# Kernel optimization log

Measured on AMD Instinct MI355X. Metric: run time of the kernel, lower is better.

## Reference

```python
import jax, jax.numpy as jnp
import numpy as np
import math

NEG_INF = -1e9  # finite sentinel, safe under fp16/bf16 too


def _maximum_path(neg_x_ent):
    """Monotonic alignment search (VITS maximum_path), batched & wavefront-parallel.

    neg_x_ent: (B, T_feats, T_text) float32. Full lengths assumed (masks all ones).
    Returns hard path (B, T_feats, T_text) in {0,1}.
    """
    B, Tf, Tt = neg_x_ent.shape
    xs_idx = jnp.arange(Tt)

    # ---- forward DP: value[y, x] = max(value[y-1, x] (x!=y), value[y-1, x-1]) + neg[y, x]
    def fwd_step(prev, inputs):
        y, row = inputs  # y scalar, row (B, Tt)
        left0 = jnp.where(y == 0, 0.0, NEG_INF)  # v_prev for x==0
        v_left = jnp.concatenate(
            [jnp.broadcast_to(left0, (B, 1)), prev[:, :-1]], axis=1)
        v_cur = jnp.where(xs_idx[None, :] == y, NEG_INF, prev)
        val = jnp.maximum(v_cur, v_left) + row
        return val, val

    init = jnp.full((B, Tt), NEG_INF, dtype=neg_x_ent.dtype)
    _, values = jax.lax.scan(
        fwd_step, init, (jnp.arange(Tf), jnp.transpose(neg_x_ent, (1, 0, 2))))
    # values: (Tf, B, Tt); values_prev[y] = values[y-1] (row -1 is -inf)
    values_prev = jnp.concatenate(
        [jnp.full((1, B, Tt), NEG_INF, values.dtype), values[:-1]], axis=0)

    # ---- backtracking from (Tf-1, Tt-1)
    def back_step(idx, inputs):
        y, vprev = inputs  # idx (B,), vprev (B, Tt)
        onehot = (xs_idx[None, :] == idx[:, None]).astype(neg_x_ent.dtype)
        v_at = jnp.take_along_axis(vprev, idx[:, None], axis=1)[:, 0]
        v_lf = jnp.take_along_axis(
            vprev, jnp.maximum(idx - 1, 0)[:, None], axis=1)[:, 0]
        move = (idx != 0) & ((idx == y) | (v_at < v_lf))
        return idx - move.astype(idx.dtype), onehot

    idx0 = jnp.full((B,), Tt - 1, dtype=jnp.int32)
    _, path_rev = jax.lax.scan(
        back_step, idx0, (jnp.arange(Tf)[::-1], values_prev[::-1]))
    path = jnp.transpose(path_rev[::-1], (1, 0, 2))  # (B, Tf, Tt)
    return path


def reference(z_p, m_p, logs_p, x_mask, y_mask):
    # Gaussian negative cross-entropy between flow latent z_p and prior (m_p, logs_p)
    s_p_sq_r = jnp.exp(-2.0 * logs_p)                              # (B, C, Tt)
    neg1 = jnp.sum(-0.5 * math.log(2.0 * math.pi) - logs_p,
                   axis=1, keepdims=True)                          # (B, 1, Tt)
    neg2 = jnp.einsum('bct,bcs->bts', -0.5 * z_p ** 2, s_p_sq_r)   # (B, Tf, Tt)
    neg3 = jnp.einsum('bct,bcs->bts', z_p, m_p * s_p_sq_r)         # (B, Tf, Tt)
    neg4 = jnp.sum(-0.5 * m_p ** 2 * s_p_sq_r, axis=1, keepdims=True)
    neg_x_ent = neg1 + neg2 + neg3 + neg4                          # (B, Tf, Tt)

    attn_mask = x_mask[:, 0, None, :] * y_mask[:, 0, :, None]      # (B, Tf, Tt)
    attn = _maximum_path(neg_x_ent) * attn_mask                    # (B, Tf, Tt)
    dur = jnp.sum(attn, axis=1)                                    # (B, Tt)
    return attn, dur, neg_x_ent


def setup_inputs() -> dict:
    key = jax.random.key(0)
    k1, k2, k3 = jax.random.split(key, 3)
    B, C, Tf, Tt = 32, 192, 2048, 512
    return {
        'z_p': jax.random.normal(k1, (B, C, Tf), dtype=jnp.float32),
        'm_p': jax.random.normal(k2, (B, C, Tt), dtype=jnp.float32),
        'logs_p': jax.random.normal(k3, (B, C, Tt), dtype=jnp.float32),
        'x_mask': jnp.ones((B, 1, Tt), dtype=jnp.float32),
        'y_mask': jnp.ones((B, 1, Tf), dtype=jnp.float32),
    }
```

## Files before the change

kernel.cpp:

```cpp
#include <hip/hip_runtime.h>
#include <math.h>

#define BATCH 32
#define CH    192
#define TFEAT 2048
#define TTXT  512
#define NEGINF (-1e9f)

#define ATTN_ELEMS ((size_t)BATCH * TFEAT * TTXT)
#define DUR_OFF    ATTN_ELEMS
#define NEG_OFF    (ATTN_ELEMS + (size_t)BATCH * TTXT)

typedef short bf16x8 __attribute__((ext_vector_type(8)));
typedef float f32x16 __attribute__((ext_vector_type(16)));

__device__ __forceinline__ void gload_lds16h(const unsigned short* g,
                                             unsigned short* l) {
  __builtin_amdgcn_global_load_lds(
      (const __attribute__((address_space(1))) void*)g,
      (__attribute__((address_space(3))) void*)l, 16, 0, 0);
}

#define VMCNT(n) asm volatile("s_waitcnt vmcnt(" #n ")" ::: "memory")

__device__ __forceinline__ unsigned short f2b16(float f) {
  unsigned u = __float_as_uint(f);
  return (unsigned short)((u + 0x7FFFu + ((u >> 16) & 1u)) >> 16);
}

__global__ __launch_bounds__(256)
void k_transA(const float* __restrict__ z_p, unsigned short* __restrict__ At2) {
  __shared__ float zt[CH][33];
  int b = blockIdx.x >> 6, tblk = blockIdx.x & 63;
  int tid = threadIdx.x;
  int t0 = tblk * 32;
  for (int i = tid; i < CH * 32; i += 256) {
    int c = i >> 5, m = i & 31;
    zt[c][m] = z_p[((size_t)b * CH + c) * TFEAT + t0 + m];
  }
  __syncthreads();
  unsigned short* out = At2 + (size_t)(b * 64 + tblk) * 24 * 512;
  for (int o = tid; o < 24 * 512; o += 256) {
    int kq = o >> 9, rem = o & 511;
    int lane = rem >> 3, j = rem & 7;
    int m = lane & 31, kh = lane >> 5;
    int k = kq * 16 + kh * 8 + j;
    float f;
    if (k < CH) f = zt[k][m];
    else { float z = zt[k - CH][m]; f = z * z; }
    out[o] = f2b16(f);
  }
}

__global__ __launch_bounds__(256)
void k_transB(const float* __restrict__ m_p, const float* __restrict__ logs_p,
              unsigned short* __restrict__ Bt2) {
  __shared__ float w1t[CH][33];
  __shared__ float w2t[CH][33];
  int b = blockIdx.x >> 4, sblk = blockIdx.x & 15;
  int tid = threadIdx.x;
  int s0 = sblk * 32;
  for (int i = tid; i < CH * 32; i += 256) {
    int c = i >> 5, n = i & 31;
    size_t idx = ((size_t)b * CH + c) * TTXT + s0 + n;
    float m = m_p[idx];
    float r = __expf(-2.0f * logs_p[idx]);
    w1t[c][n] = m * r;
    w2t[c][n] = -0.5f * r;
  }
  __syncthreads();
  unsigned short* out = Bt2 + (size_t)(b * 16 + sblk) * 24 * 512;
  for (int o = tid; o < 24 * 512; o += 256) {
    int kq = o >> 9, rem = o & 511;
    int lane = rem >> 3, j = rem & 7;
    int n = lane & 31, kh = lane >> 5;
    int k = kq * 16 + kh * 8 + j;
    float f = (k < CH) ? w1t[k][n] : w2t[k - CH][n];
    out[o] = f2b16(f);
  }
}

__global__ void k_cadd(const float* __restrict__ m_p,
                       const float* __restrict__ logs_p,
                       float* __restrict__ cadd) {
  int gid = blockIdx.x * 256 + threadIdx.x;
  int b = gid >> 9, s = gid & (TTXT - 1);
  const float* mp = m_p    + (size_t)b * CH * TTXT + s;
  const float* lp = logs_p + (size_t)b * CH * TTXT + s;
  float acc = -0.5f * 1.8378770664093453f * (float)CH;
  #pragma unroll 4
  for (int c = 0; c < CH; ++c) {
    float l = lp[(size_t)c * TTXT];
    float m = mp[(size_t)c * TTXT];
    float r = __expf(-2.0f * l);
    acc -= l + 0.5f * m * m * r;
  }
  cadd[gid] = acc;
}

__global__ __launch_bounds__(512)
void k_mf(const unsigned short* __restrict__ At2,
          const unsigned short* __restrict__ Bt2,
          const float* __restrict__ cadd,
          float* __restrict__ neg,
          unsigned short* __restrict__ negh) {
  int blk = (blockIdx.x & 7) * 128 + (blockIdx.x >> 3);
  int sb = blk & 1;
  int tb = (blk >> 1) & 15;
  int b  = blk >> 5;
  int tid = threadIdx.x, lane = tid & 63, w = tid >> 6;
  int rg = w >> 2, cg = w & 3;
  int trow0 = tb * 128 + rg * 64;
  int scol0 = sb * 256 + cg * 64;

  const unsigned short* ap0 = At2 + ((size_t)(b * 64 + (trow0 >> 5)) * 24) * 512 + lane * 8;
  const unsigned short* ap1 = ap0 + (size_t)24 * 512;
  const unsigned short* bp0 = Bt2 + ((size_t)(b * 16 + (scol0 >> 5)) * 24) * 512 + lane * 8;
  const unsigned short* bp1 = bp0 + (size_t)24 * 512;

  f32x16 acc00, acc01, acc10, acc11;
  #pragma unroll
  for (int r = 0; r < 16; ++r) { acc00[r] = 0.f; acc01[r] = 0.f; acc10[r] = 0.f; acc11[r] = 0.f; }

  bf16x8 a0A, a1A, b0A, b1A;
  bf16x8 a0B, a1B, b0B, b1B;

  auto LDA = [&](bf16x8& x0, bf16x8& x1, bf16x8& y0, bf16x8& y1, int kq) {
    x0 = *(const bf16x8*)(ap0 + (size_t)kq * 512);
    x1 = *(const bf16x8*)(ap1 + (size_t)kq * 512);
    y0 = *(const bf16x8*)(bp0 + (size_t)kq * 512);
    y1 = *(const bf16x8*)(bp1 + (size_t)kq * 512);
  };
  auto FMA = [&](bf16x8& x0, bf16x8& x1, bf16x8& y0, bf16x8& y1) {
    acc00 = __builtin_amdgcn_mfma_f32_32x32x16_bf16(x0, y0, acc00, 0, 0, 0);
    acc01 = __builtin_amdgcn_mfma_f32_32x32x16_bf16(x0, y1, acc01, 0, 0, 0);
    acc10 = __builtin_amdgcn_mfma_f32_32x32x16_bf16(x1, y0, acc10, 0, 0, 0);
    acc11 = __builtin_amdgcn_mfma_f32_32x32x16_bf16(x1, y1, acc11, 0, 0, 0);
  };

  LDA(a0A, a1A, b0A, b1A, 0);
  #pragma unroll
  for (int kq = 0; kq < 24; kq += 2) {
    LDA(a0B, a1B, b0B, b1B, kq + 1);
    FMA(a0A, a1A, b0A, b1A);
    __builtin_amdgcn_sched_barrier(0);
    if (kq + 2 < 24) LDA(a0A, a1A, b0A, b1A, kq + 2);
    FMA(a0B, a1B, b0B, b1B);
    __builtin_amdgcn_sched_barrier(0);
  }

  #pragma unroll
  for (int ti = 0; ti < 2; ++ti) {
    #pragma unroll
    for (int tj = 0; tj < 2; ++tj) {
      const f32x16& v = (ti == 0) ? ((tj == 0) ? acc00 : acc01)
                                  : ((tj == 0) ? acc10 : acc11);
      int s = scol0 + tj * 32 + (lane & 31);
      float cv = cadd[b * TTXT + s];
      int tB = trow0 + ti * 32 + 4 * (lane >> 5);
      float* np_ = neg + (size_t)b * TFEAT * TTXT + s;
      #pragma unroll
      for (int r = 0; r < 16; ++r) {
        int t = tB + (r & 3) + 8 * (r >> 2);
        float o = v[r] + cv;
        np_[(size_t)t * TTXT] = o;
        negh[(((size_t)b * 128 + (t >> 4)) * 8 + (s >> 6)) * 1024
             + (t & 15) * 64 + (s & 63)] = f2b16(o);
      }
    }
  }
}

#define KROWS 16
#define NWIN  (TFEAT / KROWS)
#define NMASKW (TTXT / KROWS)

__device__ __forceinline__ float dpp_shr1(float v) {
  return __int_as_float(__builtin_amdgcn_update_dpp(
      __float_as_int(v), __float_as_int(v), 0x138 , 0xF, 0xF, false));
}

__global__ __launch_bounds__(512, 1)
void k_dp(const unsigned short* __restrict__ negh, float* __restrict__ dur,
          int* __restrict__ idx_out, const float* __restrict__ x_mask,
          unsigned long long* __restrict__ gbits_all) {
  __shared__ unsigned short ringh[8][4][KROWS * 64];
  __shared__ float bndlds[3][8][KROWS];
  int b = blockIdx.x, tid = threadIdx.x;
  int lane = tid & 63, w = tid >> 6;
  const unsigned short* nb =
      negh + (((size_t)b * NWIN) * 8 + w) * 1024 + lane * 8;
  unsigned long long* gbits = gbits_all + (size_t)b * 8 * TFEAT;

  if (tid < 3 * 8 * KROWS) ((float*)bndlds)[tid] = NEGINF;

  auto stage = [&](int j) {
    int slot = j & 3;
    const unsigned short* s0 = nb + (size_t)j * 8 * 1024;
    gload_lds16h(s0,       &ringh[w][slot][0]);
    gload_lds16h(s0 + 512, &ringh[w][slot][512]);
  };

  stage(0); stage(1); stage(2);
  __syncthreads();

  float prev = NEGINF;
  for (int p = 0; p < NWIN + 8; ++p) {
    int i = p - w;
    if (i >= 0 && i + 3 < NWIN) { stage(i + 3); VMCNT(6); }
    else if (i >= 0) {
      int rem = NWIN - 1 - i;
      if (rem == 2)      VMCNT(4);
      else if (rem == 1) VMCNT(2);
      else               VMCNT(0);
    }
    asm volatile("s_waitcnt lgkmcnt(0)" ::: "memory");
    __builtin_amdgcn_s_barrier();
    __builtin_amdgcn_sched_barrier(0);

    if (i >= 0 && i < NWIN) {
      float s_bnd[KROWS];
      if (w > 0) {
        float v   = bndlds[i % 3][w - 1][lane & 15];
        float v15 = bndlds[(i + 2) % 3][w - 1][15];
        s_bnd[0] = __int_as_float(__builtin_amdgcn_readfirstlane(__float_as_int(v15)));
        #pragma unroll
        for (int r = 1; r < KROWS; ++r)
          s_bnd[r] = __int_as_float(__builtin_amdgcn_readlane(__float_as_int(v), r - 1));
      } else {
        #pragma unroll
        for (int r = 0; r < KROWS; ++r) s_bnd[r] = NEGINF;
        if (i == 0) s_bnd[0] = 0.0f;
      }
      float cur[KROWS];
      #pragma unroll
      for (int r = 0; r < KROWS; ++r)
        cur[r] = __uint_as_float((unsigned)ringh[w][i & 3][r * 64 + lane] << 16);

      int y0 = i * KROWS;
      bool masked = (i < NMASKW);
      unsigned keep_lo = 0, keep_hi = 0;
      float bkeep = 0.0f;
      unsigned long long andm = (w == 0) ? ~1ull : ~0ull;
      #pragma unroll
      for (int r = 0; r < KROWS; ++r) {
        float upd = dpp_shr1(prev);
        float up = (lane == 0) ? s_bnd[r] : upd;
        bool force = masked && (tid == y0 + r);
        bool gt = prev < up;
        unsigned long long m = __ballot(force || gt) & andm;
        bool mine = (lane == r);
        keep_lo = mine ? (unsigned)m : keep_lo;
        keep_hi = mine ? (unsigned)(m >> 32) : keep_hi;
        float vc = force ? NEGINF : prev;
        prev = fmaxf(vc, up) + cur[r];
        float v63 = __int_as_float(
            __builtin_amdgcn_readlane(__float_as_int(prev), 63));
        bkeep = mine ? v63 : bkeep;
      }
      if (lane < KROWS) {
        bndlds[i % 3][w][lane] = bkeep;
        gbits[(size_t)w * TFEAT + y0 + lane] =
            ((unsigned long long)keep_hi << 32) | keep_lo;
      }
    }
  }
  VMCNT(0);
  __syncthreads();

  if (tid == 0) {
    const float* xm = x_mask + (size_t)b * TTXT;
    int idx = TTXT - 1, cnt = 0;
    unsigned long long ua[16], ub[16]; int qi[16];
    #pragma unroll
    for (int q16 = 0; q16 < 16; ++q16) {
      ua[q16] = gbits[(size_t)7 * TFEAT + 2032 + q16];
      ub[q16] = gbits[(size_t)6 * TFEAT + 2032 + q16];
      qi[q16] = 7;
    }
    for (int yb = 2032; yb >= 16; yb -= 16) {
      #pragma unroll
      for (int jj = 15; jj >= 0; --jj) {
        int y = yb + jj;
        unsigned long long w64 = ((idx >> 6) == qi[jj]) ? ua[jj] : ub[jj];
        idx_out[b * TFEAT + y] = idx;
        cnt++;
        if ((w64 >> (idx & 63)) & 1ull) {
          dur[b * TTXT + idx] = (float)cnt * xm[idx];
          cnt = 0; idx--;
        }
        int q = idx >> 6;
        int qm = q > 0 ? q - 1 : 0;
        ua[jj] = gbits[(size_t)q  * TFEAT + (y - 16)];
        ub[jj] = gbits[(size_t)qm * TFEAT + (y - 16)];
        qi[jj] = q;
      }
    }
    #pragma unroll
    for (int jj = 15; jj >= 0; --jj) {
      int y = jj;
      unsigned long long w64 = ((idx >> 6) == qi[jj]) ? ua[jj] : ub[jj];
      idx_out[b * TFEAT + y] = idx;
      cnt++;
      if ((w64 >> (idx & 63)) & 1ull) {
        dur[b * TTXT + idx] = (float)cnt * xm[idx];
        cnt = 0; idx--;
      }
    }
    dur[b * TTXT] = (float)cnt * xm[0];
  }
}

__global__ void k_attn(const int* __restrict__ idx_arr,
                       const float* __restrict__ x_mask,
                       const float* __restrict__ y_mask,
                       float* __restrict__ attn) {
  size_t gid = (size_t)blockIdx.x * 256 + threadIdx.x;
  size_t e = gid << 2;
  int b = (int)(e >> 20);
  int rem = (int)(e & 1048575u);
  int y = rem >> 9;
  int x0 = rem & 511;
  int idx = idx_arr[b * TFEAT + y];
  float4 v = {0.f, 0.f, 0.f, 0.f};
  int d = idx - x0;
  if (d >= 0 && d < 4) {
    ((float*)&v)[d] = x_mask[b * TTXT + idx] * y_mask[b * TFEAT + y];
  }
  *(float4*)(attn + e) = v;
}

extern "C" void kernel_launch(void* const* d_in, const int* in_sizes, int n_in,
                              void* d_out, int out_size, void* d_ws, size_t ws_size,
                              hipStream_t stream) {
  const float* z_p    = (const float*)d_in[0];
  const float* m_p    = (const float*)d_in[1];
  const float* logs_p = (const float*)d_in[2];
  const float* x_mask = (const float*)d_in[3];
  const float* y_mask = (const float*)d_in[4];

  float* out  = (float*)d_out;
  float* attn = out;
  float* dur  = out + DUR_OFF;
  float* neg  = out + NEG_OFF;

  char* scr = (char*)attn;
  unsigned long long* gbits = (unsigned long long*)scr;
  unsigned short* negh = (unsigned short*)(scr + 4194304);
  unsigned short* At2  = (unsigned short*)(scr + 71303168);
  unsigned short* Bt2  = (unsigned short*)(scr + 121634816);

  float* cadd = (float*)d_ws;
  int*   idxa = (int*)((char*)d_ws + 65536);

  k_transA<<<BATCH * 64, 256, 0, stream>>>(z_p, At2);
  k_transB<<<BATCH * 16, 256, 0, stream>>>(m_p, logs_p, Bt2);
  k_cadd<<<(BATCH * TTXT) / 256, 256, 0, stream>>>(m_p, logs_p, cadd);
  k_mf<<<1024, 512, 0, stream>>>(At2, Bt2, cadd, neg, negh);
  k_dp<<<BATCH, 512, 0, stream>>>(negh, dur, idxa, x_mask, gbits);
  k_attn<<<(int)(ATTN_ELEMS / 4 / 256), 256, 0, stream>>>(idxa, x_mask, y_mask, attn);
}
```

Baseline: 511.8 us.

## Process two batches per block in DP kernel with 1024 threads

The DP wavefront kernel now handles two batch elements per 1024-thread block, halving the grid. Each half has its own LDS ring and boundary buffers. The intent is to interleave two independent serial DP chains on one CU to hide latency. In exchange, every barrier spans both batches, and half as many CUs are used.

```diff
diff --git a/kernel.cpp b/kernel.cpp
--- a/kernel.cpp
+++ b/kernel.cpp
@@ -180,25 +180,28 @@
       __float_as_int(v), __float_as_int(v), 0x138 , 0xF, 0xF, false));
 }
 
-__global__ __launch_bounds__(512, 1)
+__global__ __launch_bounds__(1024, 1)
 void k_dp(const unsigned short* __restrict__ negh, float* __restrict__ dur,
           int* __restrict__ idx_out, const float* __restrict__ x_mask,
           unsigned long long* __restrict__ gbits_all) {
-  __shared__ unsigned short ringh[8][4][KROWS * 64];
-  __shared__ float bndlds[3][8][KROWS];
-  int b = blockIdx.x, tid = threadIdx.x;
-  int lane = tid & 63, w = tid >> 6;
+  __shared__ unsigned short ringh[2][8][4][KROWS * 64];
+  __shared__ float bndlds[2][3][8][KROWS];
+  int tid = threadIdx.x;
+  int half = tid >> 9;
+  int tid9 = tid & 511;
+  int lane = tid & 63, w = tid9 >> 6;
+  int b = blockIdx.x * 2 + half;
   const unsigned short* nb =
       negh + (((size_t)b * NWIN) * 8 + w) * 1024 + lane * 8;
   unsigned long long* gbits = gbits_all + (size_t)b * 8 * TFEAT;
 
-  if (tid < 3 * 8 * KROWS) ((float*)bndlds)[tid] = NEGINF;
+  if (tid9 < 3 * 8 * KROWS / 4 * 4 && tid9 < 384) ((float*)bndlds[half])[tid9] = NEGINF;
 
   auto stage = [&](int j) {
     int slot = j & 3;
     const unsigned short* s0 = nb + (size_t)j * 8 * 1024;
-    gload_lds16h(s0,       &ringh[w][slot][0]);
-    gload_lds16h(s0 + 512, &ringh[w][slot][512]);
+    gload_lds16h(s0,       &ringh[half][w][slot][0]);
+    gload_lds16h(s0 + 512, &ringh[half][w][slot][512]);
   };
 
   stage(0); stage(1); stage(2);
@@ -221,8 +224,8 @@
     if (i >= 0 && i < NWIN) {
       float s_bnd[KROWS];
       if (w > 0) {
-        float v   = bndlds[i % 3][w - 1][lane & 15];
-        float v15 = bndlds[(i + 2) % 3][w - 1][15];
+        float v   = bndlds[half][i % 3][w - 1][lane & 15];
+        float v15 = bndlds[half][(i + 2) % 3][w - 1][15];
         s_bnd[0] = __int_as_float(__builtin_amdgcn_readfirstlane(__float_as_int(v15)));
         #pragma unroll
         for (int r = 1; r < KROWS; ++r)
@@ -235,7 +238,7 @@
       float cur[KROWS];
       #pragma unroll
       for (int r = 0; r < KROWS; ++r)
-        cur[r] = __uint_as_float((unsigned)ringh[w][i & 3][r * 64 + lane] << 16);
+        cur[r] = __uint_as_float((unsigned)ringh[half][w][i & 3][r * 64 + lane] << 16);
 
       int y0 = i * KROWS;
       bool masked = (i < NMASKW);
@@ -246,7 +249,7 @@
       for (int r = 0; r < KROWS; ++r) {
         float upd = dpp_shr1(prev);
         float up = (lane == 0) ? s_bnd[r] : upd;
-        bool force = masked && (tid == y0 + r);
+        bool force = masked && (tid9 == y0 + r);
         bool gt = prev < up;
         unsigned long long m = __ballot(force || gt) & andm;
         bool mine = (lane == r);
@@ -259,7 +262,7 @@
         bkeep = mine ? v63 : bkeep;
       }
       if (lane < KROWS) {
-        bndlds[i % 3][w][lane] = bkeep;
+        bndlds[half][i % 3][w][lane] = bkeep;
         gbits[(size_t)w * TFEAT + y0 + lane] =
             ((unsigned long long)keep_hi << 32) | keep_lo;
       }
@@ -268,7 +271,7 @@
   VMCNT(0);
   __syncthreads();
 
-  if (tid == 0) {
+  if (tid9 == 0) {
     const float* xm = x_mask + (size_t)b * TTXT;
     int idx = TTXT - 1, cnt = 0;
     unsigned long long ua[16], ub[16]; int qi[16];
@@ -357,6 +360,6 @@
   k_transB<<<BATCH * 16, 256, 0, stream>>>(m_p, logs_p, Bt2);
   k_cadd<<<(BATCH * TTXT) / 256, 256, 0, stream>>>(m_p, logs_p, cadd);
   k_mf<<<1024, 512, 0, stream>>>(At2, Bt2, cadd, neg, negh);
-  k_dp<<<BATCH, 512, 0, stream>>>(negh, dur, idxa, x_mask, gbits);
+  k_dp<<<BATCH / 2, 1024, 0, stream>>>(negh, dur, idxa, x_mask, gbits);
   k_attn<<<(int)(ATTN_ELEMS / 4 / 256), 256, 0, stream>>>(idxa, x_mask, y_mask, attn);
 }
```

Measured after the change: 745.5 us. 45.7% more time.
